# Kernel tuning notes

Hardware: AMD Instinct MI355X
Metric: run time of the kernel (lower is better)

The kernel has to match this reference:

```python
import jax, jax.numpy as jnp
import numpy as np

B, S, D, H = 4, 512, 1024, 16
HD = D // H
K_TOP = 8
MC_K = 8
EPS6 = 1e-6


def _affine(loc, scale, W, b):
    # Gaussian-diag affine: mu = x@W.T+b, var = scale^2 @ (W^2).T
    mu = loc @ W.T + b
    var = (scale ** 2) @ (W ** 2).T
    return mu, jnp.sqrt(var)


def _split(x):  # [B,S,D] -> [B,H,S,HD]
    return x.reshape(B, S, H, HD).transpose(0, 2, 1, 3)


def _combine(x):  # [B,H,S,HD] -> [B,S,D]
    return x.transpose(0, 2, 1, 3).reshape(B, S, D)


def _softmax_logit_normal(mu, var, excl_mask):
    # logit-normal softmax moment approximation (probit / delta method),
    # excluding masked positions (prob -> 0 there).
    adj = mu / jnp.sqrt(1.0 + (jnp.pi / 8.0) * var)
    adj = jnp.where(excl_mask, -1e9, adj)
    p = jax.nn.softmax(adj, axis=-1)
    v = (p * (1.0 - p)) ** 2 * var
    return p, v


def _forward(Q_loc, Q_scale, K_loc, K_scale, V_loc, V_scale,
             Wq, bq, Wk, bk, Wv, bv, Wo, bo, tau, eps):
    q_mu, q_sc = _affine(Q_loc, Q_scale, Wq, bq)
    k_mu, k_sc = _affine(K_loc, K_scale, Wk, bk)
    v_mu, v_sc = _affine(V_loc, V_scale, Wv, bv)

    # split heads; GaussianDiag round-trip adds 1e-6 to scale before squaring
    qm, qv = _split(q_mu), (_split(q_sc) + EPS6) ** 2
    km, kv = _split(k_mu), (_split(k_sc) + EPS6) ** 2
    vm, vv = _split(v_mu), (_split(v_sc) + EPS6) ** 2

    # bilinear moment: E[QK^T], Var[QK^T]
    S_mu = jnp.einsum('bhqd,bhkd->bhqk', qm, km)
    S_var = (jnp.einsum('bhqd,bhkd->bhqk', qm ** 2, kv)
             + jnp.einsum('bhqd,bhkd->bhqk', qv, km ** 2)
             + jnp.einsum('bhqd,bhkd->bhqk', qv, kv)) + EPS6

    s_mu = S_mu / jnp.sqrt(jnp.float32(HD))
    s_var = S_var / HD + EPS6

    l_mu = s_mu / tau
    l_var = s_var / (tau ** 2) + EPS6

    # top-k indices by mean logit
    topk_idx = jax.lax.top_k(l_mu, K_TOP)[1]  # [B,H,S,K_TOP]
    rows = jnp.arange(B * H * S)[:, None]
    mask = jnp.zeros((B * H * S, S), bool).at[rows, topk_idx.reshape(-1, K_TOP)].set(True)
    mask = mask.reshape(B, H, S, S)

    # MC-sample softmax (mc_k=8)
    std = jnp.sqrt(jnp.maximum(l_var, 1e-9))
    p_mean = jax.nn.softmax(l_mu[None] + std[None] * eps, axis=-1).mean(axis=0)

    # rest (non-top-k) logit-normal softmax moments
    rest_mean, rest_var = _softmax_logit_normal(l_mu, l_var, mask)

    top_out = jnp.where(mask, p_mean, rest_mean)
    top_out = top_out / jnp.maximum(top_out.sum(axis=-1, keepdims=True), 1e-12)

    # combine_top_rest: means add (variances do not feed the output path)
    attn_mu = top_out + rest_mean

    # linear combination with V distribution
    Y_mu = jnp.einsum('bhqk,bhkd->bhqd', attn_mu, vm)
    Y_var = jnp.einsum('bhqk,bhkd->bhqd', attn_mu ** 2, vv)
    Y_scale = jnp.sqrt(Y_var + EPS6)

    y_loc = _combine(Y_mu)
    y_scale = _combine(Y_scale) + EPS6

    out_loc = y_loc @ Wo.T + bo
    out_scale = jnp.sqrt((y_scale ** 2) @ (Wo ** 2).T)
    return out_loc, out_scale


def setup_inputs() -> dict:
    key = jax.random.key(0)
    ks = jax.random.split(key, 17)
    f32 = jnp.float32
    inp = {
        'Q_loc': jax.random.normal(ks[0], (B, S, D), f32),
        'Q_scale': jax.random.uniform(ks[1], (B, S, D), f32),
        'K_loc': jax.random.normal(ks[2], (B, S, D), f32),
        'K_scale': jax.random.uniform(ks[3], (B, S, D), f32),
        'V_loc': jax.random.normal(ks[4], (B, S, D), f32),
        'V_scale': jax.random.uniform(ks[5], (B, S, D), f32),
        'Wq': jax.random.normal(ks[6], (D, D), f32) * 0.02,
        'bq': jnp.zeros((D,), f32),
        'Wk': jax.random.normal(ks[7], (D, D), f32) * 0.02,
        'bk': jnp.zeros((D,), f32),
        'Wv': jax.random.normal(ks[8], (D, D), f32) * 0.02,
        'bv': jnp.zeros((D,), f32),
        'Wo': jax.random.normal(ks[9], (D, D), f32) * 0.02,
        'bo': jnp.zeros((D,), f32),
        'tau': jnp.array(1.0, f32),
        'eps': jax.random.normal(ks[10], (MC_K, B, H, S, S), f32),
    }
    return inp


def reference(Q_loc, Q_scale, K_loc, K_scale, V_loc, V_scale,
              Wq, bq, Wk, bk, Wv, bv, Wo, bo, tau, eps):
    return _forward(Q_loc, Q_scale, K_loc, K_scale, V_loc, V_scale,
                    Wq, bq, Wk, bk, Wv, bv, Wo, bo, tau, eps)
```

## Files before the change

kernel.cpp:

```cpp
#include <hip/hip_runtime.h>
#include <math.h>

#define B_ 4
#define S_ 512
#define D_ 1024
#define H_ 16
#define MCK 8
#define MS 2048
#define BHSS_ ((size_t)16777216)
#define BHS_  ((size_t)32768)

typedef __attribute__((ext_vector_type(8))) __bf16 bf16x8;
typedef __attribute__((ext_vector_type(4))) __bf16 bf16x4;
typedef __attribute__((ext_vector_type(4))) float f32x4;

__device__ __forceinline__ f32x4 mfma16(bf16x8 a, bf16x8 b, f32x4 c) {
  return __builtin_amdgcn_mfma_f32_16x16x32_bf16(a, b, c, 0, 0, 0);
}
__device__ __forceinline__ bf16x8 sq8(bf16x8 x) {
  bf16x8 r;
#pragma unroll
  for (int i = 0; i < 8; ++i) { float f = (float)x[i]; r[i] = (__bf16)(f * f); }
  return r;
}
__device__ __forceinline__ bf16x8 sq8s(bf16x8 h, bf16x8 l) {
  bf16x8 r;
#pragma unroll
  for (int i = 0; i < 8; ++i) { float f = (float)h[i] + (float)l[i]; r[i] = (__bf16)(f * f); }
  return r;
}
__device__ __forceinline__ float wave_max(float v) {
#pragma unroll
  for (int o = 32; o; o >>= 1) v = fmaxf(v, __shfl_xor(v, o));
  return v;
}
__device__ __forceinline__ float wave_sum(float v) {
#pragma unroll
  for (int o = 32; o; o >>= 1) v += __shfl_xor(v, o);
  return v;
}

__device__ __forceinline__ void unswz(int u, int& row, int& slot) {
  int row0 = ((u >> 2) ^ (u >> 4)) & 1;
  row = ((u >> 3) << 1) | row0;
  int s0 = (u ^ (u >> 2) ^ (u >> 4)) & 1;
  int s1 = ((u >> 1) ^ (u >> 3)) & 1;
  slot = (s1 << 1) | s0;
}
__device__ __forceinline__ int swz_el(int row, int slot) {
  return ((row * 4 + slot) ^ (row & 7)) * 8;
}
__device__ __forceinline__ void glds16(const void* gsrc, void* ldst) {
  __builtin_amdgcn_global_load_lds(
      (const __attribute__((address_space(1))) void*)gsrc,
      (__attribute__((address_space(3))) void*)ldst, 16, 0, 0);
}

__global__ __launch_bounds__(256) void conv_all(
    const float* __restrict__ l0, const float* __restrict__ s0,
    const float* __restrict__ l1, const float* __restrict__ s1,
    const float* __restrict__ l2, const float* __restrict__ s2,
    __bf16* h0, __bf16* o0, __bf16* v0,
    __bf16* h1, __bf16* o1, __bf16* v1,
    __bf16* h2, __bf16* o2, __bf16* v2,
    const float* __restrict__ w0, const float* __restrict__ w1,
    const float* __restrict__ w2, const float* __restrict__ w3,
    __bf16* wh0, __bf16* wo0, __bf16* wh1, __bf16* wo1,
    __bf16* wh2, __bf16* wo2, __bf16* wh3, __bf16* wo3)
{
  const int bid = blockIdx.x;
  if (bid < 3072) {
    const int tn = bid >> 10;
    const size_t i0 = ((size_t)(bid & 1023) * 256 + threadIdx.x) * 8;
    const float* L = tn == 0 ? l0 : tn == 1 ? l1 : l2;
    const float* S = tn == 0 ? s0 : tn == 1 ? s1 : s2;
    __bf16* Hh = tn == 0 ? h0 : tn == 1 ? h1 : h2;
    __bf16* Lo = tn == 0 ? o0 : tn == 1 ? o1 : o2;
    __bf16* V2 = tn == 0 ? v0 : tn == 1 ? v1 : v2;
    float4 x0 = *(const float4*)(L + i0), x1 = *(const float4*)(L + i0 + 4);
    float4 y0 = *(const float4*)(S + i0), y1 = *(const float4*)(S + i0 + 4);
    float xs[8] = {x0.x, x0.y, x0.z, x0.w, x1.x, x1.y, x1.z, x1.w};
    float ys[8] = {y0.x, y0.y, y0.z, y0.w, y1.x, y1.y, y1.z, y1.w};
    bf16x8 hh, ll, vv;
#pragma unroll
    for (int i = 0; i < 8; ++i) {
      __bf16 h = (__bf16)xs[i];
      hh[i] = h;
      ll[i] = (__bf16)(xs[i] - (float)h);
      vv[i] = (__bf16)(ys[i] * ys[i]);
    }
    *(bf16x8*)(Hh + i0) = hh;
    *(bf16x8*)(Lo + i0) = ll;
    *(bf16x8*)(V2 + i0) = vv;
  } else {
    const int b2 = bid - 3072;
    const int tn = b2 >> 9;
    const size_t i0 = ((size_t)(b2 & 511) * 256 + threadIdx.x) * 8;
    const float* W = tn == 0 ? w0 : tn == 1 ? w1 : tn == 2 ? w2 : w3;
    __bf16* Hh = tn == 0 ? wh0 : tn == 1 ? wh1 : tn == 2 ? wh2 : wh3;
    __bf16* Lo = tn == 0 ? wo0 : tn == 1 ? wo1 : tn == 2 ? wo2 : wo3;
    float4 x0 = *(const float4*)(W + i0), x1 = *(const float4*)(W + i0 + 4);
    float xs[8] = {x0.x, x0.y, x0.z, x0.w, x1.x, x1.y, x1.z, x1.w};
    bf16x8 hh, ll;
#pragma unroll
    for (int i = 0; i < 8; ++i) {
      __bf16 h = (__bf16)xs[i];
      hh[i] = h;
      ll[i] = (__bf16)(xs[i] - (float)h);
    }
    *(bf16x8*)(Hh + i0) = hh;
    *(bf16x8*)(Lo + i0) = ll;
  }
}

struct PArg {
  const __bf16 *Ah, *Al, *A2, *Wh, *Wl;
  const float* bias;
  __bf16 *P0, *P1, *P2, *P3;
  int epi;
};
struct PArg3 { PArg a[3]; };

#define LDSBUF 14336

__global__ __launch_bounds__(256, 2) void dgemm_qkv(PArg3 P3v)
{
  __shared__ __bf16 lds[2 * LDSBUF];
  const int lin = blockIdx.x + 8 * blockIdx.y + 256 * blockIdx.z;
  const int xcd = lin & 7;
  const int rest = lin >> 3;
  const int mi   = rest & 3;
  const int nblk = (rest >> 2) & 7;
  const int proj = rest >> 5;
  const PArg p = P3v.a[proj];
  const int m0 = (xcd + 8 * mi) * 64;
  const int n0 = nblk * 128;
  const int t = threadIdx.x, lane = t & 63, wid = t >> 6;
  int rA, sA; unswz(t, rA, sA);
  const size_t gA = (size_t)(m0 + rA) * D_ + sA * 8;
  const size_t gW0 = (size_t)(n0 + rA) * D_ + sA * 8;
  int rW1, sW1; unswz(t + 256, rW1, sW1);
  const size_t gW1 = (size_t)(n0 + rW1) * D_ + sW1 * 8;
  const int wofs = wid * 512;
  f32x4 accM[4][2] = {}; f32x4 accV[4][2] = {};
  const int fr = lane & 15, ks = lane >> 4;

  auto STAGE = [&](int buf, int k0) {
    __bf16* L = lds + buf * LDSBUF;
    glds16(p.Ah + gA + k0,  L + 0     + wofs);
    glds16(p.Al + gA + k0,  L + 2048  + wofs);
    glds16(p.A2 + gA + k0,  L + 4096  + wofs);
    glds16(p.Wh + gW0 + k0, L + 6144  + wofs);
    glds16(p.Wl + gW0 + k0, L + 10240 + wofs);
    glds16(p.Wh + gW1 + k0, L + 6144 + 2048 + wofs);
    glds16(p.Wl + gW1 + k0, L + 10240 + 2048 + wofs);
  };

  STAGE(0, 0);
  for (int tt = 0; tt < 32; ++tt) {
    const int cur = tt & 1;
    if (tt < 31) {
      STAGE(cur ^ 1, (tt + 1) * 32);
      asm volatile("s_waitcnt vmcnt(7)" ::: "memory");
    } else {
      asm volatile("s_waitcnt vmcnt(0)" ::: "memory");
    }
    __builtin_amdgcn_s_barrier();
    __builtin_amdgcn_sched_barrier(0);
    const __bf16* L = lds + cur * LDSBUF;
    bf16x8 fah[4], fal[4], fa2[4];
#pragma unroll
    for (int i = 0; i < 4; ++i) {
      int so = swz_el(i * 16 + fr, ks);
      fah[i] = *(const bf16x8*)(L + 0 + so);
      fal[i] = *(const bf16x8*)(L + 2048 + so);
      fa2[i] = *(const bf16x8*)(L + 4096 + so);
    }
#pragma unroll
    for (int j = 0; j < 2; ++j) {
      int so = swz_el(wid * 32 + j * 16 + fr, ks);
      bf16x8 fwh = *(const bf16x8*)(L + 6144 + so);
      bf16x8 fwl = *(const bf16x8*)(L + 10240 + so);
      bf16x8 fw2 = sq8s(fwh, fwl);
#pragma unroll
      for (int i = 0; i < 4; ++i) {
        accM[i][j] = mfma16(fah[i], fwh, accM[i][j]);
        accM[i][j] = mfma16(fah[i], fwl, accM[i][j]);
        accM[i][j] = mfma16(fal[i], fwh, accM[i][j]);
        accV[i][j] = mfma16(fa2[i], fw2, accV[i][j]);
      }
    }
    __builtin_amdgcn_s_barrier();
  }
  const int fq = lane >> 4;
#pragma unroll
  for (int j = 0; j < 2; ++j) {
    const int col = n0 + wid * 32 + j * 16 + fr;
    const float bcol = p.bias[col];
#pragma unroll
    for (int i = 0; i < 4; ++i) {
      const int row0 = m0 + i * 16 + fq * 4;
      f32x4 m_ = accM[i][j], v_ = accV[i][j];
      if (p.epi == 0) {
#pragma unroll
        for (int r = 0; r < 4; ++r) {
          size_t off = (size_t)(row0 + r) * D_ + col;
          float mu = m_[r] + bcol;
          __bf16 h = (__bf16)mu;
          float s = sqrtf(v_[r]) + 1e-6f;
          p.P0[off] = h;
          p.P1[off] = (__bf16)(mu - (float)h);
          p.P2[off] = (__bf16)(mu * mu);
          p.P3[off] = (__bf16)(s * s);
        }
      } else {
        const int b = row0 >> 9, ss0 = row0 & 511;
        const int hh = col >> 6, dd = col & 63;
        size_t base = ((size_t)(b * H_ + hh) * 64 + dd) * S_ + ss0;
        bf16x4 vh, vl, vq;
#pragma unroll
        for (int r = 0; r < 4; ++r) {
          float mu = m_[r] + bcol;
          __bf16 h = (__bf16)mu;
          vh[r] = h;
          vl[r] = (__bf16)(mu - (float)h);
          float s = sqrtf(v_[r]) + 1e-6f;
          vq[r] = (__bf16)(s * s);
        }
        *(bf16x4*)(p.P0 + base) = vh;
        *(bf16x4*)(p.P1 + base) = vl;
        *(bf16x4*)(p.P2 + base) = vq;
      }
    }
  }
}

__global__ __launch_bounds__(256, 2) void dgemm_o(
    const __bf16* __restrict__ Ah, const __bf16* __restrict__ Al, const __bf16* __restrict__ A2,
    const __bf16* __restrict__ Wh, const __bf16* __restrict__ Wl,
    const float* __restrict__ bias, float* __restrict__ O0, float* __restrict__ O1)
{
  __shared__ __bf16 lds[2 * LDSBUF];
  const int lin = blockIdx.x + 8 * blockIdx.y;
  const int xcd = lin & 7;
  const int rest = lin >> 3;
  const int mi   = rest & 3;
  const int nblk = rest >> 2;
  const int m0 = (xcd + 8 * mi) * 64;
  const int n0 = nblk * 128;
  const int t = threadIdx.x, lane = t & 63, wid = t >> 6;
  int rA, sA; unswz(t, rA, sA);
  const size_t gA = (size_t)(m0 + rA) * D_ + sA * 8;
  const size_t gW0 = (size_t)(n0 + rA) * D_ + sA * 8;
  int rW1, sW1; unswz(t + 256, rW1, sW1);
  const size_t gW1 = (size_t)(n0 + rW1) * D_ + sW1 * 8;
  const int wofs = wid * 512;
  f32x4 accM[4][2] = {}; f32x4 accV[4][2] = {};
  const int fr = lane & 15, ks = lane >> 4;

  auto STAGE = [&](int buf, int k0) {
    __bf16* L = lds + buf * LDSBUF;
    glds16(Ah + gA + k0,  L + 0     + wofs);
    glds16(Al + gA + k0,  L + 2048  + wofs);
    glds16(A2 + gA + k0,  L + 4096  + wofs);
    glds16(Wh + gW0 + k0, L + 6144  + wofs);
    glds16(Wl + gW0 + k0, L + 10240 + wofs);
    glds16(Wh + gW1 + k0, L + 6144 + 2048 + wofs);
    glds16(Wl + gW1 + k0, L + 10240 + 2048 + wofs);
  };

  STAGE(0, 0);
  for (int tt = 0; tt < 32; ++tt) {
    const int cur = tt & 1;
    if (tt < 31) {
      STAGE(cur ^ 1, (tt + 1) * 32);
      asm volatile("s_waitcnt vmcnt(7)" ::: "memory");
    } else {
      asm volatile("s_waitcnt vmcnt(0)" ::: "memory");
    }
    __builtin_amdgcn_s_barrier();
    __builtin_amdgcn_sched_barrier(0);
    const __bf16* L = lds + cur * LDSBUF;
    bf16x8 fah[4], fal[4], fa2[4];
#pragma unroll
    for (int i = 0; i < 4; ++i) {
      int so = swz_el(i * 16 + fr, ks);
      fah[i] = *(const bf16x8*)(L + 0 + so);
      fal[i] = *(const bf16x8*)(L + 2048 + so);
      fa2[i] = *(const bf16x8*)(L + 4096 + so);
    }
#pragma unroll
    for (int j = 0; j < 2; ++j) {
      int so = swz_el(wid * 32 + j * 16 + fr, ks);
      bf16x8 fwh = *(const bf16x8*)(L + 6144 + so);
      bf16x8 fwl = *(const bf16x8*)(L + 10240 + so);
      bf16x8 fw2 = sq8s(fwh, fwl);
#pragma unroll
      for (int i = 0; i < 4; ++i) {
        accM[i][j] = mfma16(fah[i], fwh, accM[i][j]);
        accM[i][j] = mfma16(fah[i], fwl, accM[i][j]);
        accM[i][j] = mfma16(fal[i], fwh, accM[i][j]);
        accV[i][j] = mfma16(fa2[i], fw2, accV[i][j]);
      }
    }
    __builtin_amdgcn_s_barrier();
  }
  const int fq = lane >> 4;
#pragma unroll
  for (int j = 0; j < 2; ++j) {
    const int col = n0 + wid * 32 + j * 16 + fr;
    const float bcol = bias[col];
#pragma unroll
    for (int i = 0; i < 4; ++i) {
      const int row0 = m0 + i * 16 + fq * 4;
      f32x4 m_ = accM[i][j], v_ = accV[i][j];
#pragma unroll
      for (int r = 0; r < 4; ++r) {
        size_t off = (size_t)(row0 + r) * D_ + col;
        O0[off] = m_[r] + bcol;
        O1[off] = sqrtf(v_[r]);
      }
    }
  }
}

__global__ __launch_bounds__(256) void score_mfma(
    const __bf16* __restrict__ qh, const __bf16* __restrict__ ql,
    const __bf16* __restrict__ q2, const __bf16* __restrict__ qv,
    const __bf16* __restrict__ kh, const __bf16* __restrict__ kl,
    const __bf16* __restrict__ k2, const __bf16* __restrict__ kv,
    float* __restrict__ lmu, __bf16* __restrict__ lvar,
    const float* __restrict__ taup)
{
  __shared__ __bf16 sQ[4][64][32];
  __shared__ __bf16 sK[4][64][32];
  const int t = threadIdx.x;
  const int lane = t & 63, wid = t >> 6;
  const int wm = wid >> 1, wn = wid & 1;
  const int lin = blockIdx.x + 8 * blockIdx.y + 64 * blockIdx.z;
  const int xcd = lin & 7;
  const int rest = lin >> 3;
  const int tile = rest & 63;
  const int bh = xcd + 8 * (rest >> 6);
  const int kk0 = (tile & 7) * 64, q0 = (tile >> 3) * 64;
  const int b = bh >> 4, h = bh & 15;
  const size_t hb = ((size_t)b * S_) * D_ + (size_t)h * 64;
  f32x4 accM[2][2] = {}; f32x4 accV[2][2] = {};
  const int crow = t >> 2, ccol = (t & 3) * 8;
  for (int d0 = 0; d0 < 64; d0 += 32) {
    size_t gq = hb + (size_t)(q0 + crow) * D_ + d0 + ccol;
    size_t gk = hb + (size_t)(kk0 + crow) * D_ + d0 + ccol;
    bf16x8 a0 = *(const bf16x8*)(qh + gq);
    bf16x8 a1 = *(const bf16x8*)(ql + gq);
    bf16x8 a2 = *(const bf16x8*)(q2 + gq);
    bf16x8 a3 = *(const bf16x8*)(qv + gq);
    bf16x8 b0 = *(const bf16x8*)(kh + gk);
    bf16x8 b1 = *(const bf16x8*)(kl + gk);
    bf16x8 b2 = *(const bf16x8*)(k2 + gk);
    bf16x8 b3 = *(const bf16x8*)(kv + gk);
    __syncthreads();
    *(bf16x8*)&sQ[0][crow][ccol] = a0;
    *(bf16x8*)&sQ[1][crow][ccol] = a1;
    *(bf16x8*)&sQ[2][crow][ccol] = a2;
    *(bf16x8*)&sQ[3][crow][ccol] = a3;
    *(bf16x8*)&sK[0][crow][ccol] = b0;
    *(bf16x8*)&sK[1][crow][ccol] = b1;
    *(bf16x8*)&sK[2][crow][ccol] = b2;
    *(bf16x8*)&sK[3][crow][ccol] = b3;
    __syncthreads();
    const int fr = lane & 15, kc = (lane >> 4) * 8;
    bf16x8 fqh[2], fql[2], fq2[2], fqv[2];
#pragma unroll
    for (int i = 0; i < 2; ++i) {
      int r = wm * 32 + i * 16 + fr;
      fqh[i] = *(const bf16x8*)&sQ[0][r][kc];
      fql[i] = *(const bf16x8*)&sQ[1][r][kc];
      fq2[i] = *(const bf16x8*)&sQ[2][r][kc];
      fqv[i] = *(const bf16x8*)&sQ[3][r][kc];
    }
#pragma unroll
    for (int j = 0; j < 2; ++j) {
      int r = wn * 32 + j * 16 + fr;
      bf16x8 fkh = *(const bf16x8*)&sK[0][r][kc];
      bf16x8 fkl = *(const bf16x8*)&sK[1][r][kc];
      bf16x8 fk2 = *(const bf16x8*)&sK[2][r][kc];
      bf16x8 fkv = *(const bf16x8*)&sK[3][r][kc];
#pragma unroll
      for (int i = 0; i < 2; ++i) {
        accM[i][j] = mfma16(fqh[i], fkh, accM[i][j]);
        accM[i][j] = mfma16(fqh[i], fkl, accM[i][j]);
        accM[i][j] = mfma16(fql[i], fkh, accM[i][j]);
        accV[i][j] = mfma16(fq2[i], fkv, accV[i][j]);
        accV[i][j] = mfma16(fqv[i], fk2, accV[i][j]);
        accV[i][j] = mfma16(fqv[i], fkv, accV[i][j]);
      }
    }
  }
  const float itau = 1.0f / *taup;
  const int fr = lane & 15, fq = lane >> 4;
#pragma unroll
  for (int i = 0; i < 2; ++i)
#pragma unroll
    for (int j = 0; j < 2; ++j) {
      const int col = kk0 + wn * 32 + j * 16 + fr;
      const int row0 = q0 + wm * 32 + i * 16 + fq * 4;
      f32x4 m_ = accM[i][j], v_ = accV[i][j];
#pragma unroll
      for (int r = 0; r < 4; ++r) {
        size_t off = ((size_t)bh * S_ + row0 + r) * S_ + col;
        lmu[off] = m_[r] * 0.125f * itau;
        float lv = ((v_[r] + 1e-6f) * (1.0f / 64.0f) + 1e-6f) * itau * itau + 1e-6f;
        lvar[off] = (__bf16)lv;
      }
    }
}

__global__ __launch_bounds__(256) void attn_kernel(
    const float* __restrict__ lmu, const __bf16* __restrict__ lvar,
    const float* __restrict__ eps, __bf16* __restrict__ ah, __bf16* __restrict__ al)
{
  const int wid = threadIdx.x >> 6;
  const int lane = threadIdx.x & 63;
  const size_t r = (size_t)blockIdx.x * 4 + wid;
  const float* mrow = lmu + r * S_;
  const __bf16* vrow = lvar + r * S_;
  const int c0 = lane * 4;
  float mu[8], va[8], sd[8];
  {
    float4 m0 = *(const float4*)(mrow + c0);
    float4 m1 = *(const float4*)(mrow + 256 + c0);
    mu[0] = m0.x; mu[1] = m0.y; mu[2] = m0.z; mu[3] = m0.w;
    mu[4] = m1.x; mu[5] = m1.y; mu[6] = m1.z; mu[7] = m1.w;
    bf16x4 v0 = *(const bf16x4*)(vrow + c0);
    bf16x4 v1 = *(const bf16x4*)(vrow + 256 + c0);
#pragma unroll
    for (int i = 0; i < 4; ++i) { va[i] = (float)v0[i]; va[4 + i] = (float)v1[i]; }
  }
#pragma unroll
  for (int i = 0; i < 8; ++i) sd[i] = sqrtf(fmaxf(va[i], 1e-9f));
  unsigned sel = 0;
  float x[8];
#pragma unroll
  for (int i = 0; i < 8; ++i) x[i] = mu[i];
  for (int tsel = 0; tsel < 8; ++tsel) {
    float bv = -INFINITY; int bi = 0x7fffffff;
#pragma unroll
    for (int i = 0; i < 8; ++i) {
      int gi = (i < 4) ? (c0 + i) : (256 + c0 + i - 4);
      if (x[i] > bv || (x[i] == bv && gi < bi)) { bv = x[i]; bi = gi; }
    }
    for (int o = 32; o; o >>= 1) {
      float ov = __shfl_xor(bv, o); int oi = __shfl_xor(bi, o);
      if (ov > bv || (ov == bv && oi < bi)) { bv = ov; bi = oi; }
    }
    int half = bi >> 8;
    int rem = bi & 255;
    if ((rem >> 2) == lane) {
      int slot = (rem & 3) + 4 * half;
      sel |= 1u << slot;
      x[slot] = -INFINITY;
    }
  }
  float pacc[8] = {0, 0, 0, 0, 0, 0, 0, 0};
  for (int mc = 0; mc < MCK; ++mc) {
    const float* ep = eps + (size_t)mc * BHSS_ + r * S_;
    float4 e0 = *(const float4*)(ep + c0);
    float4 e1 = *(const float4*)(ep + 256 + c0);
    float xv[8];
    xv[0] = mu[0] + sd[0] * e0.x; xv[1] = mu[1] + sd[1] * e0.y;
    xv[2] = mu[2] + sd[2] * e0.z; xv[3] = mu[3] + sd[3] * e0.w;
    xv[4] = mu[4] + sd[4] * e1.x; xv[5] = mu[5] + sd[5] * e1.y;
    xv[6] = mu[6] + sd[6] * e1.z; xv[7] = mu[7] + sd[7] * e1.w;
    float m = -INFINITY;
#pragma unroll
    for (int i = 0; i < 8; ++i) m = fmaxf(m, xv[i]);
    m = wave_max(m);
    float e[8], zs = 0.f;
#pragma unroll
    for (int i = 0; i < 8; ++i) { e[i] = __expf(xv[i] - m); zs += e[i]; }
    zs = wave_sum(zs);
    float inv = 1.0f / zs;
#pragma unroll
    for (int i = 0; i < 8; ++i) pacc[i] += e[i] * inv;
  }
  float adj[8];
#pragma unroll
  for (int i = 0; i < 8; ++i) {
    float a = mu[i] / sqrtf(1.0f + 0.39269908169872414f * va[i]);
    adj[i] = ((sel >> i) & 1u) ? -1e9f : a;
  }
  float m2 = -INFINITY;
#pragma unroll
  for (int i = 0; i < 8; ++i) m2 = fmaxf(m2, adj[i]);
  m2 = wave_max(m2);
  float e2[8], z2 = 0.f;
#pragma unroll
  for (int i = 0; i < 8; ++i) { e2[i] = __expf(adj[i] - m2); z2 += e2[i]; }
  z2 = wave_sum(z2);
  float inv2 = 1.0f / z2;
  float rest[8], tout[8], s = 0.f;
#pragma unroll
  for (int i = 0; i < 8; ++i) {
    rest[i] = e2[i] * inv2;
    tout[i] = ((sel >> i) & 1u) ? pacc[i] * 0.125f : rest[i];
    s += tout[i];
  }
  s = wave_sum(s);
  float rn = 1.0f / fmaxf(s, 1e-12f);
  bf16x4 oh0, oh1, ol0, ol1;
#pragma unroll
  for (int i = 0; i < 4; ++i) {
    float o = tout[i] * rn + rest[i];
    __bf16 h = (__bf16)o;
    oh0[i] = h; ol0[i] = (__bf16)(o - (float)h);
    float o1 = tout[4 + i] * rn + rest[4 + i];
    __bf16 h1 = (__bf16)o1;
    oh1[i] = h1; ol1[i] = (__bf16)(o1 - (float)h1);
  }
  *(bf16x4*)(ah + r * S_ + c0) = oh0;
  *(bf16x4*)(ah + r * S_ + 256 + c0) = oh1;
  *(bf16x4*)(al + r * S_ + c0) = ol0;
  *(bf16x4*)(al + r * S_ + 256 + c0) = ol1;
}

__global__ __launch_bounds__(256) void pv_mfma(
    const __bf16* __restrict__ ah_, const __bf16* __restrict__ al_,
    const __bf16* __restrict__ vTh, const __bf16* __restrict__ vTl,
    const __bf16* __restrict__ vTv,
    __bf16* __restrict__ yh, __bf16* __restrict__ yl, __bf16* __restrict__ ys2)
{
  __shared__ __bf16 sA[2][64][32];
  __shared__ __bf16 sV[3][64][32];
  const int t = threadIdx.x;
  const int lane = t & 63, wid = t >> 6;
  const int wm = wid >> 1, wn = wid & 1;
  const int lin = blockIdx.x + 8 * blockIdx.y;
  const int xcd = lin & 7;
  const int rest = lin >> 3;
  const int q0 = (rest & 7) * 64;
  const int bh = xcd + 8 * (rest >> 3);
  const int b = bh >> 4, h = bh & 15;
  const __bf16* Ah = ah_ + (size_t)bh * S_ * S_;
  const __bf16* Al = al_ + (size_t)bh * S_ * S_;
  const __bf16* Vh = vTh + (size_t)bh * 64 * S_;
  const __bf16* Vl = vTl + (size_t)bh * 64 * S_;
  const __bf16* Vv = vTv + (size_t)bh * 64 * S_;
  f32x4 accM[2][2] = {}; f32x4 accV[2][2] = {};
  const int crow = t >> 2, ccol = (t & 3) * 8;
  for (int k0 = 0; k0 < S_; k0 += 32) {
    size_t gA = (size_t)(q0 + crow) * S_ + k0 + ccol;
    size_t gV = (size_t)crow * S_ + k0 + ccol;
    bf16x8 a0 = *(const bf16x8*)(Ah + gA);
    bf16x8 a1 = *(const bf16x8*)(Al + gA);
    bf16x8 v0 = *(const bf16x8*)(Vh + gV);
    bf16x8 v1 = *(const bf16x8*)(Vl + gV);
    bf16x8 v2 = *(const bf16x8*)(Vv + gV);
    __syncthreads();
    *(bf16x8*)&sA[0][crow][ccol] = a0;
    *(bf16x8*)&sA[1][crow][ccol] = a1;
    *(bf16x8*)&sV[0][crow][ccol] = v0;
    *(bf16x8*)&sV[1][crow][ccol] = v1;
    *(bf16x8*)&sV[2][crow][ccol] = v2;
    __syncthreads();
    const int fr = lane & 15, kc = (lane >> 4) * 8;
    bf16x8 fah[2], fal[2], fa2[2];
#pragma unroll
    for (int i = 0; i < 2; ++i) {
      int rr = wm * 32 + i * 16 + fr;
      fah[i] = *(const bf16x8*)&sA[0][rr][kc];
      fal[i] = *(const bf16x8*)&sA[1][rr][kc];
      fa2[i] = sq8(fah[i]);
    }
#pragma unroll
    for (int j = 0; j < 2; ++j) {
      int rr = wn * 32 + j * 16 + fr;
      bf16x8 fvh = *(const bf16x8*)&sV[0][rr][kc];
      bf16x8 fvl = *(const bf16x8*)&sV[1][rr][kc];
      bf16x8 fvv = *(const bf16x8*)&sV[2][rr][kc];
#pragma unroll
      for (int i = 0; i < 2; ++i) {
        accM[i][j] = mfma16(fah[i], fvh, accM[i][j]);
        accM[i][j] = mfma16(fah[i], fvl, accM[i][j]);
        accM[i][j] = mfma16(fal[i], fvh, accM[i][j]);
        accV[i][j] = mfma16(fa2[i], fvv, accV[i][j]);
      }
    }
  }
  const int fr = lane & 15, fq = lane >> 4;
#pragma unroll
  for (int i = 0; i < 2; ++i)
#pragma unroll
    for (int j = 0; j < 2; ++j) {
      const int col = h * 64 + wn * 32 + j * 16 + fr;
      const int row0 = b * S_ + q0 + wm * 32 + i * 16 + fq * 4;
      f32x4 m_ = accM[i][j], v_ = accV[i][j];
#pragma unroll
      for (int r = 0; r < 4; ++r) {
        size_t off = (size_t)(row0 + r) * D_ + col;
        float mu = m_[r];
        __bf16 hh = (__bf16)mu;
        float ss = sqrtf(v_[r] + 1e-6f) + 1e-6f;
        yh[off] = hh;
        yl[off] = (__bf16)(mu - (float)hh);
        ys2[off] = (__bf16)(ss * ss);
      }
    }
}

extern "C" void kernel_launch(void* const* d_in, const int* in_sizes, int n_in,
                              void* d_out, int out_size, void* d_ws, size_t ws_size,
                              hipStream_t stream)
{
  const float* Qloc = (const float*)d_in[0];
  const float* Qsc  = (const float*)d_in[1];
  const float* Kloc = (const float*)d_in[2];
  const float* Ksc  = (const float*)d_in[3];
  const float* Vloc = (const float*)d_in[4];
  const float* Vsc  = (const float*)d_in[5];
  const float* Wq = (const float*)d_in[6];  const float* bq = (const float*)d_in[7];
  const float* Wk = (const float*)d_in[8];  const float* bk = (const float*)d_in[9];
  const float* Wv = (const float*)d_in[10]; const float* bv = (const float*)d_in[11];
  const float* Wo = (const float*)d_in[12]; const float* bo = (const float*)d_in[13];
  const float* tau = (const float*)d_in[14];
  const float* eps = (const float*)d_in[15];

  const size_t P = (size_t)MS * D_;
  const size_t DD = (size_t)D_ * D_;
  char* w = (char*)d_ws;
  auto carve = [&](size_t bytes) -> char* {
    char* p = w; w += (bytes + 255) & ~(size_t)255; return p;
  };
  __bf16* cQh = (__bf16*)carve(P * 2); __bf16* cQl = (__bf16*)carve(P * 2); __bf16* cQ2 = (__bf16*)carve(P * 2);
  __bf16* cKh = (__bf16*)carve(P * 2); __bf16* cKl = (__bf16*)carve(P * 2); __bf16* cK2 = (__bf16*)carve(P * 2);
  __bf16* cVh = (__bf16*)carve(P * 2); __bf16* cVl = (__bf16*)carve(P * 2); __bf16* cV2 = (__bf16*)carve(P * 2);
  __bf16* wqh = (__bf16*)carve(DD * 2); __bf16* wql = (__bf16*)carve(DD * 2);
  __bf16* wkh = (__bf16*)carve(DD * 2); __bf16* wkl = (__bf16*)carve(DD * 2);
  __bf16* wvh = (__bf16*)carve(DD * 2); __bf16* wvl = (__bf16*)carve(DD * 2);
  __bf16* woh = (__bf16*)carve(DD * 2); __bf16* wol = (__bf16*)carve(DD * 2);
  __bf16* qmh = (__bf16*)carve(P * 2); __bf16* qml = (__bf16*)carve(P * 2);
  __bf16* qm2 = (__bf16*)carve(P * 2); __bf16* qmv = (__bf16*)carve(P * 2);
  __bf16* kmh = (__bf16*)carve(P * 2); __bf16* kml = (__bf16*)carve(P * 2);
  __bf16* km2 = (__bf16*)carve(P * 2); __bf16* kmv = (__bf16*)carve(P * 2);
  __bf16* vTh = (__bf16*)carve(P * 2); __bf16* vTl = (__bf16*)carve(P * 2); __bf16* vTv = (__bf16*)carve(P * 2);
  float*  lmu = (float*)carve(BHSS_ * 4);
  __bf16* lvr = (__bf16*)carve(BHSS_ * 2);
  __bf16* ath = (__bf16*)carve(BHSS_ * 2);
  __bf16* atl = (__bf16*)carve(BHSS_ * 2);
  __bf16* yh = (__bf16*)carve(P * 2); __bf16* yl = (__bf16*)carve(P * 2); __bf16* ys2 = (__bf16*)carve(P * 2);
  float* out_loc = (float*)d_out;
  float* out_sc  = out_loc + P;

  dim3 blk(256);
  conv_all<<<5120, blk, 0, stream>>>(Qloc, Qsc, Kloc, Ksc, Vloc, Vsc,
                                     cQh, cQl, cQ2, cKh, cKl, cK2, cVh, cVl, cV2,
                                     Wq, Wk, Wv, Wo,
                                     wqh, wql, wkh, wkl, wvh, wvl, woh, wol);
  PArg3 pq;
  pq.a[0] = PArg{cQh, cQl, cQ2, wqh, wql, bq, qmh, qml, qm2, qmv, 0};
  pq.a[1] = PArg{cKh, cKl, cK2, wkh, wkl, bk, kmh, kml, km2, kmv, 0};
  pq.a[2] = PArg{cVh, cVl, cV2, wvh, wvl, bv, vTh, vTl, vTv, nullptr, 1};
  dgemm_qkv<<<dim3(8, 32, 3), blk, 0, stream>>>(pq);
  score_mfma<<<dim3(8, 8, 64), blk, 0, stream>>>(qmh, qml, qm2, qmv, kmh, kml, km2, kmv, lmu, lvr, tau);
  attn_kernel<<<dim3((unsigned)(BHS_ / 4)), blk, 0, stream>>>(lmu, lvr, eps, ath, atl);
  pv_mfma<<<dim3(8, 64), blk, 0, stream>>>(ath, atl, vTh, vTl, vTv, yh, yl, ys2);
  dgemm_o<<<dim3(8, 32), blk, 0, stream>>>(yh, yl, ys2, woh, wol, bo, out_loc, out_sc);
}
```

Before: 348.1 us.

## Use async global-to-LDS loads with swizzling and double buffering in score and PV kernels

Both score_mfma and pv_mfma now stage tiles through global_load_lds straight into swizzled LDS instead of loading to registers and storing. score_mfma loads the whole 64-wide head dimension at once, and pv_mfma double-buffers K-chunks so the next chunk's loads overlap the current MFMA work. The aim is to cut register staging, bank conflicts and load latency stalls. In exchange it relies on manual vmcnt waits and barriers being correct, and score_mfma now uses 64KB of LDS, which limits occupancy.

```diff
diff --git a/kernel.cpp b/kernel.cpp
--- a/kernel.cpp
+++ b/kernel.cpp
@@ -49,6 +49,13 @@
 }
 __device__ __forceinline__ int swz_el(int row, int slot) {
   return ((row * 4 + slot) ^ (row & 7)) * 8;
+}
+__device__ __forceinline__ int swz8_el(int row, int slot) {
+  return ((row * 8 + slot) ^ (row & 7)) * 8;
+}
+__device__ __forceinline__ void unswz8(int u, int& row, int& slot) {
+  row = u >> 3;
+  slot = (u & 7) ^ (row & 7);
 }
 __device__ __forceinline__ void glds16(const void* gsrc, void* ldst) {
   __builtin_amdgcn_global_load_lds(
@@ -324,7 +331,7 @@
   }
 }
 
-__global__ __launch_bounds__(256) void score_mfma(
+__global__ __launch_bounds__(256, 2) void score_mfma(
     const __bf16* __restrict__ qh, const __bf16* __restrict__ ql,
     const __bf16* __restrict__ q2, const __bf16* __restrict__ qv,
     const __bf16* __restrict__ kh, const __bf16* __restrict__ kl,
@@ -332,8 +339,7 @@
     float* __restrict__ lmu, __bf16* __restrict__ lvar,
     const float* __restrict__ taup)
 {
-  __shared__ __bf16 sQ[4][64][32];
-  __shared__ __bf16 sK[4][64][32];
+  __shared__ __bf16 S[32768];
   const int t = threadIdx.x;
   const int lane = t & 63, wid = t >> 6;
   const int wm = wid >> 1, wn = wid & 1;
@@ -345,59 +351,58 @@
   const int kk0 = (tile & 7) * 64, q0 = (tile >> 3) * 64;
   const int b = bh >> 4, h = bh & 15;
   const size_t hb = ((size_t)b * S_) * D_ + (size_t)h * 64;
+  {
+    int r0, s0, r1, s1;
+    unswz8(t, r0, s0);
+    unswz8(t + 256, r1, s1);
+    const __bf16* qa[4] = {qh, ql, q2, qv};
+    const __bf16* ka[4] = {kh, kl, k2, kv};
+    const int wofs = wid * 512;
+#pragma unroll
+    for (int a = 0; a < 4; ++a) {
+      glds16(qa[a] + hb + (size_t)(q0 + r0) * D_ + s0 * 8, S + a * 4096 + wofs);
+      glds16(qa[a] + hb + (size_t)(q0 + r1) * D_ + s1 * 8, S + a * 4096 + 2048 + wofs);
+      glds16(ka[a] + hb + (size_t)(kk0 + r0) * D_ + s0 * 8, S + 16384 + a * 4096 + wofs);
+      glds16(ka[a] + hb + (size_t)(kk0 + r1) * D_ + s1 * 8, S + 16384 + a * 4096 + 2048 + wofs);
+    }
+  }
+  asm volatile("s_waitcnt vmcnt(0)" ::: "memory");
+  __builtin_amdgcn_s_barrier();
+  __builtin_amdgcn_sched_barrier(0);
+
   f32x4 accM[2][2] = {}; f32x4 accV[2][2] = {};
-  const int crow = t >> 2, ccol = (t & 3) * 8;
-  for (int d0 = 0; d0 < 64; d0 += 32) {
-    size_t gq = hb + (size_t)(q0 + crow) * D_ + d0 + ccol;
-    size_t gk = hb + (size_t)(kk0 + crow) * D_ + d0 + ccol;
-    bf16x8 a0 = *(const bf16x8*)(qh + gq);
-    bf16x8 a1 = *(const bf16x8*)(ql + gq);
-    bf16x8 a2 = *(const bf16x8*)(q2 + gq);
-    bf16x8 a3 = *(const bf16x8*)(qv + gq);
-    bf16x8 b0 = *(const bf16x8*)(kh + gk);
-    bf16x8 b1 = *(const bf16x8*)(kl + gk);
-    bf16x8 b2 = *(const bf16x8*)(k2 + gk);
-    bf16x8 b3 = *(const bf16x8*)(kv + gk);
-    __syncthreads();
-    *(bf16x8*)&sQ[0][crow][ccol] = a0;
-    *(bf16x8*)&sQ[1][crow][ccol] = a1;
-    *(bf16x8*)&sQ[2][crow][ccol] = a2;
-    *(bf16x8*)&sQ[3][crow][ccol] = a3;
-    *(bf16x8*)&sK[0][crow][ccol] = b0;
-    *(bf16x8*)&sK[1][crow][ccol] = b1;
-    *(bf16x8*)&sK[2][crow][ccol] = b2;
-    *(bf16x8*)&sK[3][crow][ccol] = b3;
-    __syncthreads();
-    const int fr = lane & 15, kc = (lane >> 4) * 8;
-    bf16x8 fqh[2], fql[2], fq2[2], fqv[2];
+  const int fr = lane & 15, fq = lane >> 4;
+#pragma unroll
+  for (int ds = 0; ds < 2; ++ds) {
+    const int slot = ds * 4 + fq;
+    bf16x8 fqh_[2], fql_[2], fq2_[2], fqv_[2];
 #pragma unroll
     for (int i = 0; i < 2; ++i) {
-      int r = wm * 32 + i * 16 + fr;
-      fqh[i] = *(const bf16x8*)&sQ[0][r][kc];
-      fql[i] = *(const bf16x8*)&sQ[1][r][kc];
-      fq2[i] = *(const bf16x8*)&sQ[2][r][kc];
-      fqv[i] = *(const bf16x8*)&sQ[3][r][kc];
+      int off = swz8_el(wm * 32 + i * 16 + fr, slot);
+      fqh_[i] = *(const bf16x8*)(S + 0 * 4096 + off);
+      fql_[i] = *(const bf16x8*)(S + 1 * 4096 + off);
+      fq2_[i] = *(const bf16x8*)(S + 2 * 4096 + off);
+      fqv_[i] = *(const bf16x8*)(S + 3 * 4096 + off);
     }
 #pragma unroll
     for (int j = 0; j < 2; ++j) {
-      int r = wn * 32 + j * 16 + fr;
-      bf16x8 fkh = *(const bf16x8*)&sK[0][r][kc];
-      bf16x8 fkl = *(const bf16x8*)&sK[1][r][kc];
-      bf16x8 fk2 = *(const bf16x8*)&sK[2][r][kc];
-      bf16x8 fkv = *(const bf16x8*)&sK[3][r][kc];
+      int koff = swz8_el(wn * 32 + j * 16 + fr, slot);
+      bf16x8 fkh_ = *(const bf16x8*)(S + 16384 + 0 * 4096 + koff);
+      bf16x8 fkl_ = *(const bf16x8*)(S + 16384 + 1 * 4096 + koff);
+      bf16x8 fk2_ = *(const bf16x8*)(S + 16384 + 2 * 4096 + koff);
+      bf16x8 fkv_ = *(const bf16x8*)(S + 16384 + 3 * 4096 + koff);
 #pragma unroll
       for (int i = 0; i < 2; ++i) {
-        accM[i][j] = mfma16(fqh[i], fkh, accM[i][j]);
-        accM[i][j] = mfma16(fqh[i], fkl, accM[i][j]);
-        accM[i][j] = mfma16(fql[i], fkh, accM[i][j]);
-        accV[i][j] = mfma16(fq2[i], fkv, accV[i][j]);
-        accV[i][j] = mfma16(fqv[i], fk2, accV[i][j]);
-        accV[i][j] = mfma16(fqv[i], fkv, accV[i][j]);
+        accM[i][j] = mfma16(fqh_[i], fkh_, accM[i][j]);
+        accM[i][j] = mfma16(fqh_[i], fkl_, accM[i][j]);
+        accM[i][j] = mfma16(fql_[i], fkh_, accM[i][j]);
+        accV[i][j] = mfma16(fq2_[i], fkv_, accV[i][j]);
+        accV[i][j] = mfma16(fqv_[i], fk2_, accV[i][j]);
+        accV[i][j] = mfma16(fqv_[i], fkv_, accV[i][j]);
       }
     }
   }
   const float itau = 1.0f / *taup;
-  const int fr = lane & 15, fq = lane >> 4;
 #pragma unroll
   for (int i = 0; i < 2; ++i)
 #pragma unroll
@@ -523,14 +528,14 @@
   *(bf16x4*)(al + r * S_ + 256 + c0) = ol1;
 }
 
-__global__ __launch_bounds__(256) void pv_mfma(
+#define PVBUF 10240
+__global__ __launch_bounds__(256, 2) void pv_mfma(
     const __bf16* __restrict__ ah_, const __bf16* __restrict__ al_,
     const __bf16* __restrict__ vTh, const __bf16* __restrict__ vTl,
     const __bf16* __restrict__ vTv,
     __bf16* __restrict__ yh, __bf16* __restrict__ yl, __bf16* __restrict__ ys2)
 {
-  __shared__ __bf16 sA[2][64][32];
-  __shared__ __bf16 sV[3][64][32];
+  __shared__ __bf16 lds[2 * PVBUF];
   const int t = threadIdx.x;
   const int lane = t & 63, wid = t >> 6;
   const int wm = wid >> 1, wn = wid & 1;
@@ -545,38 +550,48 @@
   const __bf16* Vh = vTh + (size_t)bh * 64 * S_;
   const __bf16* Vl = vTl + (size_t)bh * 64 * S_;
   const __bf16* Vv = vTv + (size_t)bh * 64 * S_;
+  int rA, sA; unswz(t, rA, sA);
+  const size_t gAo = (size_t)(q0 + rA) * S_ + sA * 8;
+  const size_t gVo = (size_t)rA * S_ + sA * 8;
+  const int wofs = wid * 512;
   f32x4 accM[2][2] = {}; f32x4 accV[2][2] = {};
-  const int crow = t >> 2, ccol = (t & 3) * 8;
-  for (int k0 = 0; k0 < S_; k0 += 32) {
-    size_t gA = (size_t)(q0 + crow) * S_ + k0 + ccol;
-    size_t gV = (size_t)crow * S_ + k0 + ccol;
-    bf16x8 a0 = *(const bf16x8*)(Ah + gA);
-    bf16x8 a1 = *(const bf16x8*)(Al + gA);
-    bf16x8 v0 = *(const bf16x8*)(Vh + gV);
-    bf16x8 v1 = *(const bf16x8*)(Vl + gV);
-    bf16x8 v2 = *(const bf16x8*)(Vv + gV);
-    __syncthreads();
-    *(bf16x8*)&sA[0][crow][ccol] = a0;
-    *(bf16x8*)&sA[1][crow][ccol] = a1;
-    *(bf16x8*)&sV[0][crow][ccol] = v0;
-    *(bf16x8*)&sV[1][crow][ccol] = v1;
-    *(bf16x8*)&sV[2][crow][ccol] = v2;
-    __syncthreads();
-    const int fr = lane & 15, kc = (lane >> 4) * 8;
+  const int fr = lane & 15, ks = lane >> 4;
+
+  auto STAGE = [&](int buf, int k0) {
+    __bf16* L = lds + buf * PVBUF;
+    glds16(Ah + gAo + k0, L + 0    + wofs);
+    glds16(Al + gAo + k0, L + 2048 + wofs);
+    glds16(Vh + gVo + k0, L + 4096 + wofs);
+    glds16(Vl + gVo + k0, L + 6144 + wofs);
+    glds16(Vv + gVo + k0, L + 8192 + wofs);
+  };
+
+  STAGE(0, 0);
+  for (int tt = 0; tt < 16; ++tt) {
+    const int cur = tt & 1;
+    if (tt < 15) {
+      STAGE(cur ^ 1, (tt + 1) * 32);
+      asm volatile("s_waitcnt vmcnt(5)" ::: "memory");
+    } else {
+      asm volatile("s_waitcnt vmcnt(0)" ::: "memory");
+    }
+    __builtin_amdgcn_s_barrier();
+    __builtin_amdgcn_sched_barrier(0);
+    const __bf16* L = lds + cur * PVBUF;
     bf16x8 fah[2], fal[2], fa2[2];
 #pragma unroll
     for (int i = 0; i < 2; ++i) {
-      int rr = wm * 32 + i * 16 + fr;
-      fah[i] = *(const bf16x8*)&sA[0][rr][kc];
-      fal[i] = *(const bf16x8*)&sA[1][rr][kc];
+      int so = swz_el(wm * 32 + i * 16 + fr, ks);
+      fah[i] = *(const bf16x8*)(L + 0 + so);
+      fal[i] = *(const bf16x8*)(L + 2048 + so);
       fa2[i] = sq8(fah[i]);
     }
 #pragma unroll
     for (int j = 0; j < 2; ++j) {
-      int rr = wn * 32 + j * 16 + fr;
-      bf16x8 fvh = *(const bf16x8*)&sV[0][rr][kc];
-      bf16x8 fvl = *(const bf16x8*)&sV[1][rr][kc];
-      bf16x8 fvv = *(const bf16x8*)&sV[2][rr][kc];
+      int so = swz_el(wn * 32 + j * 16 + fr, ks);
+      bf16x8 fvh = *(const bf16x8*)(L + 4096 + so);
+      bf16x8 fvl = *(const bf16x8*)(L + 6144 + so);
+      bf16x8 fvv = *(const bf16x8*)(L + 8192 + so);
 #pragma unroll
       for (int i = 0; i < 2; ++i) {
         accM[i][j] = mfma16(fah[i], fvh, accM[i][j]);
@@ -585,8 +600,9 @@
         accV[i][j] = mfma16(fa2[i], fvv, accV[i][j]);
       }
     }
-  }
-  const int fr = lane & 15, fq = lane >> 4;
+    __builtin_amdgcn_s_barrier();
+  }
+  const int fq = lane >> 4;
 #pragma unroll
   for (int i = 0; i < 2; ++i)
 #pragma unroll
```

Result: no change. 342.6 us, median of 2 (-1.6%).
